# Optimization experiments

Measured on AMD Instinct MI355X. Metric: run time of the kernel, lower is better.

Reference implementation:

```python
import jax, jax.numpy as jnp
import numpy as np

H = 1024
B_SZ = 4
L = 2048


def setup_inputs() -> dict:
    key = jax.random.key(0)
    ks = jax.random.split(key, 7)
    s_in = 1.0 / np.sqrt(H)
    x = jax.random.normal(ks[0], (B_SZ, L, H), dtype=jnp.float32)
    # torch nn.Linear weights: (out_features, in_features)
    W_proj = jax.random.uniform(ks[1], (4 * H, H), minval=-s_in, maxval=s_in, dtype=jnp.float32)
    W_delta = jax.random.uniform(ks[2], (H, H), minval=-s_in, maxval=s_in, dtype=jnp.float32)
    b_delta = jax.random.uniform(ks[3], (H,), minval=-s_in, maxval=s_in, dtype=jnp.float32)
    A = 0.02 * jax.random.normal(ks[4], (1, 1, H), dtype=jnp.float32)
    Bp = 0.02 * jax.random.normal(ks[5], (1, H, 1), dtype=jnp.float32)
    D = jnp.ones((1,), dtype=jnp.float32)
    return {"x": x, "W_proj": W_proj, "A": A, "Bp": Bp, "D": D, "W_delta": W_delta, "b_delta": b_delta}


def reference(x, W_proj, A, Bp, D, W_delta, b_delta):
    # x: (b, l, h)
    h = x.shape[-1]
    proj = x @ W_proj.T                                   # (b, l, 4h)
    delta, Bs, Cs, residual = jnp.split(proj, 4, axis=-1) # each (b, l, h)
    delta = jax.nn.softplus(delta @ W_delta.T + b_delta)  # (b, l, h)
    A1 = A[0, 0]       # (h,)
    B1 = Bp[0, :, 0]   # (h,)
    # discretization: dA[b,h,l] = exp(delta*A)[b,l,h] * B1[h] (n-dim of Bp has size 1)
    dA = jnp.exp(delta * A1) * B1                         # (b, l, h), layout transposed vs torch
    # dB[b,h,0,l] = cumsum_l(delta[b,l,h] * B1[h])
    dB = jnp.cumsum(delta * B1, axis=1)                   # (b, l, h)
    # selective_scan: y[b,h,l] = sum_n (dA[b,h,l]*u[b,h,n] + dB[b,h,0,l]) * C[b,h,n]
    # sum over n distributes: y = dA * sum_n(u*C) + dB * sum_n(C)
    uC = jnp.sum(x * Cs, axis=1, keepdims=True)           # (b, 1, h)
    Csum = jnp.sum(Cs, axis=1, keepdims=True)             # (b, 1, h)
    y = dA * uC + dB * Csum                               # (b, l, h)
    return y + residual * D
```

## Files before the change

kernel.cpp:

```cpp
#include <hip/hip_runtime.h>
#include <hip/hip_bf16.h>
#include <cstdint>

#define H 1024
#define BSZ 4
#define LSEQ 2048
#define M_TOT (BSZ*LSEQ)
#define NCH2 128
#define LCH2 16

typedef __attribute__((ext_vector_type(4))) float  f32x4;
typedef __attribute__((ext_vector_type(2))) float  f32x2;
typedef __attribute__((ext_vector_type(8))) __bf16 bf16x8;
typedef __attribute__((ext_vector_type(4))) __bf16 bf16x4;
typedef __attribute__((ext_vector_type(2))) __bf16 bf16x2;

typedef __attribute__((address_space(1))) unsigned int as1_u32;
typedef __attribute__((address_space(3))) unsigned int as3_u32;

__device__ __forceinline__ void gld_lds16(const void* g, const void* l) {
    as1_u32* gp = reinterpret_cast<as1_u32*>((uintptr_t)g);
    as3_u32* lp = reinterpret_cast<as3_u32*>((uint32_t)(uintptr_t)l);
    __builtin_amdgcn_global_load_lds(gp, lp, 16, 0, 0);
}

__device__ __forceinline__ float softplus_fast(float f) {
    return fmaxf(f, 0.f) + __logf(1.f + __expf(-fabsf(f)));
}

#define BAR()    asm volatile("s_barrier" ::: "memory")
#define WAIT6()  asm volatile("s_waitcnt vmcnt(6)" ::: "memory")
#define WAIT0()  asm volatile("s_waitcnt vmcnt(0)" ::: "memory")

__global__ __launch_bounds__(256) void wfuse_gemm(
    const __bf16* __restrict__ A,
    const __bf16* __restrict__ B,
    __bf16* __restrict__ O)
{
    __shared__ __align__(16) __bf16 lds[2*4096];
    const int tid  = threadIdx.x;
    const int lane = tid & 63;
    const int wid  = tid >> 6;
    const int l15  = lane & 15;
    const int quad = lane >> 4;
    const int row0 = blockIdx.y * 64;
    const int col0 = blockIdx.x * 64;

    const __bf16* Asrc = A + (size_t)(row0 + (tid >> 2)) * 1024 + (tid & 3) * 8;
    const __bf16* Bsrc = B + (size_t)(col0 + (tid >> 2)) * 1024 + (tid & 3) * 8;
    const int ldst = (tid >> 2) * 32 + (tid & 3) * 8;

    auto stage = [&](int buf, int kt) {
        gld_lds16(Asrc + kt * 32, lds + buf * 4096 + ldst);
        gld_lds16(Bsrc + kt * 32, lds + buf * 4096 + 2048 + ldst);
    };

    f32x4 acc[4] = {};
    stage(0, 0);
#pragma unroll 2
    for (int kt = 0; kt < 32; ++kt) {
        __syncthreads();
        if (kt + 1 < 32) stage((kt + 1) & 1, kt + 1);
        const __bf16* base = lds + (kt & 1) * 4096;
        bf16x8 a = *(const bf16x8*)(base + (wid * 16 + l15) * 32 + quad * 8);
        bf16x8 b[4];
#pragma unroll
        for (int j = 0; j < 4; ++j)
            b[j] = *(const bf16x8*)(base + 2048 + (j * 16 + l15) * 32 + quad * 8);
#pragma unroll
        for (int j = 0; j < 4; ++j)
            acc[j] = __builtin_amdgcn_mfma_f32_16x16x32_bf16(a, b[j], acc[j], 0, 0, 0);
    }

    const int rowb = row0 + wid * 16 + quad * 4;
#pragma unroll
    for (int j = 0; j < 4; ++j) {
        const int col = col0 + j * 16 + l15;
#pragma unroll
        for (int r = 0; r < 4; ++r)
            O[(size_t)(rowb + r) * H + col] = (__bf16)acc[j][r];
    }
}


#define STA(b,u,kt) gld_lds16(Asrc + (size_t)((u)*64)*H + (kt)*64, \
                              lds + (b)*24576 + (u)*4096 + lwb)
#define STB(b,u,kt) gld_lds16(Bsrc + (size_t)((u)*64)*H + (kt)*64, \
                              lds + (b)*24576 + 16384 + (u)*4096 + lwb)
#define STAGE6(b,kt) do { STA(b,0,kt); STA(b,1,kt); STA(b,2,kt); STA(b,3,kt); \
                          STB(b,0,kt); STB(b,1,kt); } while(0)

#define TILE(bc,bn,kn,DS,WAITMAC) do {                                        \
    WAITMAC();                                                                \
    BAR();                                                                    \
    { const __bf16* base_ = lds + (bc)*24576;                                 \
      _Pragma("unroll")                                                       \
      for (int i_ = 0; i_ < 4; ++i_) {                                        \
          af0[i_] = *(const bf16x8*)(base_ + aoff[i_]);                       \
          bf0[i_] = *(const bf16x8*)(base_ + boff[i_]);                       \
      }                                                                       \
      _Pragma("unroll")                                                       \
      for (int i_ = 0; i_ < 4; ++i_) {                                        \
          af1[i_] = *(const bf16x8*)(base_ + (aoff[i_] ^ 32));                \
          bf1[i_] = *(const bf16x8*)(base_ + (boff[i_] ^ 32));                \
      } }                                                                     \
    if (DS) STAGE6(bn, kn);                                                   \
    __builtin_amdgcn_s_setprio(1);                                            \
    _Pragma("unroll")                                                         \
    for (int i_ = 0; i_ < 4; ++i_)                                            \
    _Pragma("unroll")                                                         \
    for (int j_ = 0; j_ < 4; ++j_)                                            \
        acc[i_][j_] = __builtin_amdgcn_mfma_f32_16x16x32_bf16(                \
            af0[i_], bf0[j_], acc[i_][j_], 0, 0, 0);                          \
    _Pragma("unroll")                                                         \
    for (int i_ = 0; i_ < 4; ++i_)                                            \
    _Pragma("unroll")                                                         \
    for (int j_ = 0; j_ < 4; ++j_)                                            \
        acc[i_][j_] = __builtin_amdgcn_mfma_f32_16x16x32_bf16(                \
            af1[i_], bf1[j_], acc[i_][j_], 0, 0, 0);                          \
    __builtin_amdgcn_s_setprio(0);                                            \
} while(0)

__global__ __launch_bounds__(512, 2) void gemm256b(
    const __bf16* __restrict__ A,
    const __bf16* __restrict__ B,
    __bf16* __restrict__ O0,
    __bf16* __restrict__ O2,
    const __bf16* __restrict__ xb,
    const float* __restrict__ bias,
    float* __restrict__ pD,
    float* __restrict__ pUp,
    float* __restrict__ pCp)
{
    __shared__ __align__(16) __bf16 lds[73728];

    const int tid  = threadIdx.x;
    const int lane = tid & 63;
    const int wid  = tid >> 6;
    const int l15  = lane & 15;
    const int quad = lane >> 4;
    const int wrv  = (wid >> 1) * 64;
    const int wcv  = (wid & 1) * 64;

    const int bid = blockIdx.x;
    const int swz = (bid & 7) * 96 + (bid >> 3);
    const int bx = swz % 24;
    const int by = swz / 24;
    const int row0 = by * 256;
    const int col0 = bx * 128;

    const int lg = (tid & 7) ^ ((tid >> 3) & 7);
    const __bf16* Asrc = A + (size_t)(row0 + (tid >> 3)) * H + lg * 8;
    const __bf16* Bsrc = B + (size_t)(col0 + (tid >> 3)) * H + lg * 8;
    const int lwb = wid * 512;

    int aoff[4], boff[4];
#pragma unroll
    for (int i = 0; i < 4; ++i)
        aoff[i] = (wrv + i*16 + l15)*64 + ((quad ^ (l15 & 7)) << 3);
#pragma unroll
    for (int j = 0; j < 4; ++j)
        boff[j] = 16384 + (wcv + j*16 + l15)*64 + ((quad ^ (l15 & 7)) << 3);

    f32x4 acc[4][4] = {};
    bf16x8 af0[4], bf0[4], af1[4], bf1[4];

    STAGE6(0, 0);
    STAGE6(1, 1);

#pragma unroll 1
    for (int g = 0; g < 4; ++g) {
        TILE(0, 2, 3*g + 2, 1, WAIT6);
        TILE(1, 0, 3*g + 3, 1, WAIT6);
        TILE(2, 1, 3*g + 4, 1, WAIT6);
    }
    TILE(0, 2, 14, 1, WAIT6);
    TILE(1, 0, 15, 1, WAIT6);
    TILE(2, 0,  0, 0, WAIT6);
    TILE(0, 0,  0, 0, WAIT0);
    __syncthreads();

    const int seg   = col0 >> 10;
    const int cbase = col0 & 1023;
    const int colb  = cbase + wcv + l15;
    const int rowb  = row0 + wrv + quad*4;

    if (seg == 0) {
        const int chunk16 = (row0 + wrv) >> 4;
#pragma unroll
        for (int j = 0; j < 4; ++j) {
            const int col = colb + j*16;
            const float bv = bias[col];
#pragma unroll
            for (int i = 0; i < 4; ++i) {
                float s = 0.f;
#pragma unroll
                for (int r = 0; r < 4; ++r) {
                    float f = softplus_fast(acc[i][j][r] + bv);
                    O0[(size_t)(rowb + i*16 + r) * H + col] = (__bf16)f;
                    s += f;
                }
                s += __shfl_down(s, 32); s += __shfl_down(s, 16);
                if (quad == 0) pD[(size_t)(chunk16 + i)*H + col] = s;
            }
        }
    } else if (seg == 2) {
#pragma unroll
        for (int i = 0; i < 4; ++i)
#pragma unroll
            for (int j = 0; j < 4; ++j) {
                const int col = colb + j*16;
#pragma unroll
                for (int r = 0; r < 4; ++r)
                    O2[(size_t)(rowb + i*16 + r) * H + col] = (__bf16)acc[i][j][r];
            }
    } else {
#pragma unroll
        for (int i = 0; i < 4; ++i)
#pragma unroll
            for (int j = 0; j < 4; ++j) {
                const int lcol = wcv + j*16 + l15;
#pragma unroll
                for (int r = 0; r < 4; ++r) {
                    const int lrow = wrv + i*16 + quad*4 + r;
                    lds[lrow*128 + (((lcol>>3) ^ (lrow&15)) << 3) + (lcol&7)]
                        = (__bf16)acc[i][j][r];
                }
            }
        __syncthreads();
        const int g = tid >> 4, oct = tid & 15;
        const int gc0 = cbase + oct*8;
        float su[8] = {}, sc[8] = {};
#pragma unroll
        for (int rr = 0; rr < 8; ++rr) {
            const int lrow = g*8 + rr;
            bf16x8 cv = *(const bf16x8*)(lds + lrow*128 +
                                         ((oct ^ (lrow&15)) << 3));
            bf16x8 xv = *(const bf16x8*)(xb + (size_t)(row0 + lrow)*H + gc0);
#pragma unroll
            for (int q = 0; q < 8; ++q) {
                float c = (float)cv[q];
                su[q] += (float)xv[q] * c;
                sc[q] += c;
            }
        }
        float* pf = reinterpret_cast<float*>(lds);
        __syncthreads();
#pragma unroll
        for (int q = 0; q < 8; ++q) {
            pf[g*128 + oct*8 + q]        = su[q];
            pf[4096 + g*128 + oct*8 + q] = sc[q];
        }
        __syncthreads();
        const int col = tid & 127;
        const int rb  = (tid >> 7) & 1;
        const int arr = tid >> 8;
        float s = 0.f;
#pragma unroll
        for (int g2 = 0; g2 < 16; ++g2)
            s += pf[arr*4096 + (rb*16 + g2)*128 + col];
        float* dst = arr ? pCp : pUp;
        dst[(size_t)((row0 >> 7) + rb)*H + cbase + col] = s;
    }
}

#define XB 8192
#define PB 2048
#define DB 1024
#define TB 256
__global__ void cast_kernel(const float* __restrict__ x,
                            const float* __restrict__ Wp,
                            const float* __restrict__ Wd,
                            __bf16* __restrict__ xb,
                            __bf16* __restrict__ Wpb,
                            __bf16* __restrict__ Wdb,
                            __bf16* __restrict__ Wp1T)
{
    __shared__ __bf16 tlds[64*65];
    const int t = threadIdx.x;
    const int bidx = blockIdx.x;

    if (bidx < XB + PB + DB) {
        const f32x4* src; __bf16* dst; int si, di;
        if (bidx < XB) {
            int i = bidx*256 + t;
            src = (const f32x4*)x;  si = i; dst = xb;  di = i;
        } else if (bidx < XB + PB) {
            int j = (bidx - XB)*256 + t;
            int row = j >> 8, cf = j & 255;
            src = (const f32x4*)Wp; si = (2048 + row)*256 + cf;
            dst = Wpb; di = (1024 + row)*256 + cf;
        } else {
            int j = (bidx - XB - PB)*256 + t;
            src = (const f32x4*)Wd; si = j; dst = Wdb; di = j;
        }
        f32x4 v = src[si];
        bf16x4 o = { (__bf16)v[0], (__bf16)v[1], (__bf16)v[2], (__bf16)v[3] };
        *(bf16x4*)(dst + (size_t)di*4) = o;
    } else {
        int tt = bidx - (XB + PB + DB);
        int ty = tt >> 4, tx = tt & 15;
        int rb = t >> 4, cb = t & 15;
#pragma unroll
        for (int rr = 0; rr < 4; ++rr) {
            int row = rb*4 + rr;
            f32x4 v = *(const f32x4*)(Wp + (size_t)(ty*64 + row)*1024 + tx*64 + cb*4);
#pragma unroll
            for (int q = 0; q < 4; ++q)
                tlds[row*65 + cb*4 + q] = (__bf16)v[q];
        }
        __syncthreads();
#pragma unroll
        for (int rr = 0; rr < 4; ++rr) {
            int kk = rb*4 + rr;
            bf16x4 o = { tlds[(cb*4+0)*65 + kk], tlds[(cb*4+1)*65 + kk],
                         tlds[(cb*4+2)*65 + kk], tlds[(cb*4+3)*65 + kk] };
            *(bf16x4*)(Wp1T + (size_t)(tx*64 + kk)*1024 + ty*64 + cb*4) = o;
        }
    }
}

__global__ __launch_bounds__(128) void final_kernel(
                             const __bf16* __restrict__ delta,
                             const __bf16* __restrict__ res,
                             const float* __restrict__ pD,
                             const float* __restrict__ pUp,
                             const float* __restrict__ pCp,
                             const float* __restrict__ Av,
                             const float* __restrict__ Bv,
                             const float* __restrict__ Dv,
                             float* __restrict__ out)
{
    const int c = blockIdx.x, b = blockIdx.z;
    const int h0 = blockIdx.y * 256 + threadIdx.x * 2;
    float run0 = 0.f, run1 = 0.f;
#pragma unroll 4
    for (int cp = 0; cp < c; ++cp) {
        f32x2 v = *(const f32x2*)(pD + (size_t)(b*NCH2 + cp)*H + h0);
        run0 += v[0]; run1 += v[1];
    }
    float uc0 = 0.f, uc1 = 0.f, cs0 = 0.f, cs1 = 0.f;
#pragma unroll
    for (int i = 0; i < 16; ++i) {
        f32x2 u = *(const f32x2*)(pUp + (b*16 + i)*H + h0);
        f32x2 s = *(const f32x2*)(pCp + (b*16 + i)*H + h0);
        uc0 += u[0]; uc1 += u[1]; cs0 += s[0]; cs1 += s[1];
    }
    const f32x2 a1 = *(const f32x2*)(Av + h0);
    const f32x2 b1 = *(const f32x2*)(Bv + h0);
    const float dd = Dv[0];
    size_t base = ((size_t)(b*LSEQ + c*LCH2)) * H + h0;
#pragma unroll 4
    for (int l = 0; l < LCH2; ++l) {
        size_t idx = base + (size_t)l * H;
        bf16x2 dv2 = *(const bf16x2*)(delta + idx);
        bf16x2 rs2 = *(const bf16x2*)(res + idx);
        float d0 = (float)dv2[0], d1v = (float)dv2[1];
        run0 += d0; run1 += d1v;
        f32x2 o;
        o[0] = __expf(d0*a1[0])*b1[0]*uc0 + run0*b1[0]*cs0 + (float)rs2[0]*dd;
        o[1] = __expf(d1v*a1[1])*b1[1]*uc1 + run1*b1[1]*cs1 + (float)rs2[1]*dd;
        *(f32x2*)(out + idx) = o;
    }
}

extern "C" void kernel_launch(void* const* d_in, const int* in_sizes, int n_in,
                              void* d_out, int out_size, void* d_ws, size_t ws_size,
                              hipStream_t stream)
{
    (void)in_sizes; (void)n_in; (void)out_size; (void)ws_size;
    const float* x  = (const float*)d_in[0];
    const float* Wp = (const float*)d_in[1];
    const float* Av = (const float*)d_in[2];
    const float* Bv = (const float*)d_in[3];
    const float* Dv = (const float*)d_in[4];
    const float* Wd = (const float*)d_in[5];
    const float* bd = (const float*)d_in[6];
    float* out = (float*)d_out;

    char* ws = (char*)d_ws;
    size_t o = 0;
    auto alloc = [&](size_t bytes) {
        void* p = ws + o; o += (bytes + 255) & ~(size_t)255; return p;
    };
    __bf16* xb   = (__bf16*)alloc((size_t)M_TOT * H * 2);
    __bf16* Wpb  = (__bf16*)alloc((size_t)3072 * H * 2);
    __bf16* Wdb  = (__bf16*)alloc((size_t)H * H * 2);
    __bf16* Wp1T = (__bf16*)alloc((size_t)H * H * 2);
    __bf16* resb = (__bf16*)alloc((size_t)M_TOT * H * 2);
    __bf16* db   = (__bf16*)alloc((size_t)M_TOT * H * 2);
    float*  pD   = (float*)alloc((size_t)BSZ * NCH2 * H * 4);
    float*  pUp  = (float*)alloc((size_t)64 * H * 4);
    float*  pCp  = (float*)alloc((size_t)64 * H * 4);

    cast_kernel<<<XB + PB + DB + TB, 256, 0, stream>>>(
        x, Wp, Wd, xb, Wpb, Wdb, Wp1T);
    wfuse_gemm<<<dim3(16, 16), 256, 0, stream>>>(Wdb, Wp1T, Wpb);
    gemm256b<<<dim3(768), 512, 0, stream>>>(
        xb, Wpb, db, resb, xb, bd, pD, pUp, pCp);
    final_kernel<<<dim3(NCH2, 4, BSZ), 128, 0, stream>>>(db, resb, pD, pUp, pCp,
                                                         Av, Bv, Dv, out);
}
```

Baseline: 192.9 us.

## Split K across wave pairs in GEMM with LDS reduction of partial accumulators

Reorganizes the 8-wave GEMM so each wave pair splits the 64-wide K slice in half, with every wave computing a 128x64 output subtile (8x4 MFMA tiles) over half of K. This gives more A/B fragment reuse per LDS read (12 fragment loads for 32 MFMAs instead of 16 for 32). At the end, the upper-K waves write their partial accumulators to LDS and the lower-K waves add them, and only those waves run the epilogue. The cost is double the accumulator registers (128 floats), which threatens occupancy at 2 blocks per CU, plus an extra LDS reduction pass and an epilogue that uses half the waves.

After: 214.8 us. 11.4% more time.

```diff
diff --git a/kernel.cpp b/kernel.cpp
--- a/kernel.cpp
+++ b/kernel.cpp
@@ -95,29 +95,19 @@
     BAR();                                                                    \
     { const __bf16* base_ = lds + (bc)*24576;                                 \
       _Pragma("unroll")                                                       \
-      for (int i_ = 0; i_ < 4; ++i_) {                                        \
-          af0[i_] = *(const bf16x8*)(base_ + aoff[i_]);                       \
-          bf0[i_] = *(const bf16x8*)(base_ + boff[i_]);                       \
-      }                                                                       \
+      for (int j_ = 0; j_ < 4; ++j_)                                          \
+          bf[j_] = *(const bf16x8*)(base_ + boff[j_]);                        \
       _Pragma("unroll")                                                       \
-      for (int i_ = 0; i_ < 4; ++i_) {                                        \
-          af1[i_] = *(const bf16x8*)(base_ + (aoff[i_] ^ 32));                \
-          bf1[i_] = *(const bf16x8*)(base_ + (boff[i_] ^ 32));                \
-      } }                                                                     \
+      for (int i_ = 0; i_ < 8; ++i_)                                          \
+          af[i_] = *(const bf16x8*)(base_ + aoff[i_]); }                      \
     if (DS) STAGE6(bn, kn);                                                   \
     __builtin_amdgcn_s_setprio(1);                                            \
     _Pragma("unroll")                                                         \
-    for (int i_ = 0; i_ < 4; ++i_)                                            \
+    for (int i_ = 0; i_ < 8; ++i_)                                            \
     _Pragma("unroll")                                                         \
     for (int j_ = 0; j_ < 4; ++j_)                                            \
         acc[i_][j_] = __builtin_amdgcn_mfma_f32_16x16x32_bf16(                \
-            af0[i_], bf0[j_], acc[i_][j_], 0, 0, 0);                          \
-    _Pragma("unroll")                                                         \
-    for (int i_ = 0; i_ < 4; ++i_)                                            \
-    _Pragma("unroll")                                                         \
-    for (int j_ = 0; j_ < 4; ++j_)                                            \
-        acc[i_][j_] = __builtin_amdgcn_mfma_f32_16x16x32_bf16(                \
-            af1[i_], bf1[j_], acc[i_][j_], 0, 0, 0);                          \
+            af[i_], bf[j_], acc[i_][j_], 0, 0, 0);                            \
     __builtin_amdgcn_s_setprio(0);                                            \
 } while(0)
 
@@ -139,8 +129,9 @@
     const int wid  = tid >> 6;
     const int l15  = lane & 15;
     const int quad = lane >> 4;
-    const int wrv  = (wid >> 1) * 64;
-    const int wcv  = (wid & 1) * 64;
+    const int kh = wid & 1;
+    const int nn = (wid >> 1) & 1;
+    const int mm = wid >> 2;
 
     const int bid = blockIdx.x;
     const int swz = (bid & 7) * 96 + (bid >> 3);
@@ -154,16 +145,16 @@
     const __bf16* Bsrc = B + (size_t)(col0 + (tid >> 3)) * H + lg * 8;
     const int lwb = wid * 512;
 
-    int aoff[4], boff[4];
-#pragma unroll
-    for (int i = 0; i < 4; ++i)
-        aoff[i] = (wrv + i*16 + l15)*64 + ((quad ^ (l15 & 7)) << 3);
+    int aoff[8], boff[4];
+#pragma unroll
+    for (int i = 0; i < 8; ++i)
+        aoff[i] = (mm*128 + i*16 + l15)*64 + (((kh*4 + quad) ^ (l15 & 7)) << 3);
 #pragma unroll
     for (int j = 0; j < 4; ++j)
-        boff[j] = 16384 + (wcv + j*16 + l15)*64 + ((quad ^ (l15 & 7)) << 3);
-
-    f32x4 acc[4][4] = {};
-    bf16x8 af0[4], bf0[4], af1[4], bf1[4];
+        boff[j] = 16384 + (nn*64 + j*16 + l15)*64 + (((kh*4 + quad) ^ (l15 & 7)) << 3);
+
+    f32x4 acc[8][4] = {};
+    bf16x8 af[8], bf[4];
 
     STAGE6(0, 0);
     STAGE6(1, 1);
@@ -180,53 +171,81 @@
     TILE(0, 0,  0, 0, WAIT0);
     __syncthreads();
 
+    float* pf = reinterpret_cast<float*>(lds);
+    const int pairb = (wid >> 1) * 8192;
+    if (kh == 1) {
+#pragma unroll
+        for (int i = 0; i < 8; ++i)
+#pragma unroll
+            for (int j = 0; j < 4; ++j)
+                *(f32x4*)(pf + pairb + (i*4 + j)*256 + lane*4) = acc[i][j];
+    }
+    __syncthreads();
+    if (kh == 0) {
+#pragma unroll
+        for (int i = 0; i < 8; ++i)
+#pragma unroll
+            for (int j = 0; j < 4; ++j) {
+                f32x4 v = *(const f32x4*)(pf + pairb + (i*4 + j)*256 + lane*4);
+                acc[i][j][0] += v[0]; acc[i][j][1] += v[1];
+                acc[i][j][2] += v[2]; acc[i][j][3] += v[3];
+            }
+    }
+
     const int seg   = col0 >> 10;
     const int cbase = col0 & 1023;
-    const int colb  = cbase + wcv + l15;
-    const int rowb  = row0 + wrv + quad*4;
+    const int colb  = cbase + nn*64 + l15;
+    const int rowb  = row0 + mm*128 + quad*4;
 
     if (seg == 0) {
-        const int chunk16 = (row0 + wrv) >> 4;
-#pragma unroll
-        for (int j = 0; j < 4; ++j) {
-            const int col = colb + j*16;
-            const float bv = bias[col];
-#pragma unroll
-            for (int i = 0; i < 4; ++i) {
-                float s = 0.f;
-#pragma unroll
-                for (int r = 0; r < 4; ++r) {
-                    float f = softplus_fast(acc[i][j][r] + bv);
-                    O0[(size_t)(rowb + i*16 + r) * H + col] = (__bf16)f;
-                    s += f;
-                }
-                s += __shfl_down(s, 32); s += __shfl_down(s, 16);
-                if (quad == 0) pD[(size_t)(chunk16 + i)*H + col] = s;
-            }
-        }
-    } else if (seg == 2) {
-#pragma unroll
-        for (int i = 0; i < 4; ++i)
+        if (kh == 0) {
+            const int chunk16 = (row0 + mm*128) >> 4;
 #pragma unroll
             for (int j = 0; j < 4; ++j) {
                 const int col = colb + j*16;
-#pragma unroll
-                for (int r = 0; r < 4; ++r)
-                    O2[(size_t)(rowb + i*16 + r) * H + col] = (__bf16)acc[i][j][r];
-            }
-    } else {
-#pragma unroll
-        for (int i = 0; i < 4; ++i)
-#pragma unroll
-            for (int j = 0; j < 4; ++j) {
-                const int lcol = wcv + j*16 + l15;
-#pragma unroll
-                for (int r = 0; r < 4; ++r) {
-                    const int lrow = wrv + i*16 + quad*4 + r;
-                    lds[lrow*128 + (((lcol>>3) ^ (lrow&15)) << 3) + (lcol&7)]
-                        = (__bf16)acc[i][j][r];
+                const float bv = bias[col];
+#pragma unroll
+                for (int i = 0; i < 8; ++i) {
+                    float s = 0.f;
+#pragma unroll
+                    for (int r = 0; r < 4; ++r) {
+                        float f = softplus_fast(acc[i][j][r] + bv);
+                        O0[(size_t)(rowb + i*16 + r) * H + col] = (__bf16)f;
+                        s += f;
+                    }
+                    s += __shfl_down(s, 32); s += __shfl_down(s, 16);
+                    if (quad == 0) pD[(size_t)(chunk16 + i)*H + col] = s;
                 }
             }
+        }
+    } else if (seg == 2) {
+        if (kh == 0) {
+#pragma unroll
+            for (int i = 0; i < 8; ++i)
+#pragma unroll
+                for (int j = 0; j < 4; ++j) {
+                    const int col = colb + j*16;
+#pragma unroll
+                    for (int r = 0; r < 4; ++r)
+                        O2[(size_t)(rowb + i*16 + r) * H + col] = (__bf16)acc[i][j][r];
+                }
+        }
+    } else {
+        __syncthreads();
+        if (kh == 0) {
+#pragma unroll
+            for (int i = 0; i < 8; ++i)
+#pragma unroll
+                for (int j = 0; j < 4; ++j) {
+                    const int lcol = nn*64 + j*16 + l15;
+#pragma unroll
+                    for (int r = 0; r < 4; ++r) {
+                        const int lrow = mm*128 + i*16 + quad*4 + r;
+                        lds[lrow*128 + (((lcol>>3) ^ (lrow&15)) << 3) + (lcol&7)]
+                            = (__bf16)acc[i][j][r];
+                    }
+                }
+        }
         __syncthreads();
         const int g = tid >> 4, oct = tid & 15;
         const int gc0 = cbase + oct*8;
@@ -244,7 +263,6 @@
                 sc[q] += c;
             }
         }
-        float* pf = reinterpret_cast<float*>(lds);
         __syncthreads();
 #pragma unroll
         for (int q = 0; q < 8; ++q) {
```

## Load B operand directly into registers, staging only A through LDS

Applied to the files above, without the earlier changes.

The main GEMM now streams only the A tile through a triple-buffered LDS pipeline. The B fragments are loaded straight from global memory into two ping-pong register sets, one k-step ahead. This cuts LDS size (and possibly raises occupancy) and removes the B LDS reads and their bank traffic. In exchange it adds register pressure, and it relies on uncoalesced per-wave global loads of B whose latency is covered only by the vmcnt waits.

Result: slower. 268.6 us (+39.3%).

```diff
diff --git a/kernel.cpp b/kernel.cpp
--- a/kernel.cpp
+++ b/kernel.cpp
@@ -29,7 +29,7 @@
 }
 
 #define BAR()    asm volatile("s_barrier" ::: "memory")
-#define WAIT6()  asm volatile("s_waitcnt vmcnt(6)" ::: "memory")
+#define WAIT4()  asm volatile("s_waitcnt vmcnt(4)" ::: "memory")
 #define WAIT0()  asm volatile("s_waitcnt vmcnt(0)" ::: "memory")
 
 __global__ __launch_bounds__(256) void wfuse_gemm(
@@ -83,41 +83,46 @@
 }
 
 
-#define STA(b,u,kt) gld_lds16(Asrc + (size_t)((u)*64)*H + (kt)*64, \
-                              lds + (b)*24576 + (u)*4096 + lwb)
-#define STB(b,u,kt) gld_lds16(Bsrc + (size_t)((u)*64)*H + (kt)*64, \
-                              lds + (b)*24576 + 16384 + (u)*4096 + lwb)
-#define STAGE6(b,kt) do { STA(b,0,kt); STA(b,1,kt); STA(b,2,kt); STA(b,3,kt); \
-                          STB(b,0,kt); STB(b,1,kt); } while(0)
-
-#define TILE(bc,bn,kn,DS,WAITMAC) do {                                        \
+#define STA4(b,kt) do {                                                       \
+    gld_lds16(Asrc + (size_t)  0*H + (kt)*64, lds + (b)*16384 +         lwb); \
+    gld_lds16(Asrc + (size_t) 64*H + (kt)*64, lds + (b)*16384 +  4096 + lwb); \
+    gld_lds16(Asrc + (size_t)128*H + (kt)*64, lds + (b)*16384 +  8192 + lwb); \
+    gld_lds16(Asrc + (size_t)192*H + (kt)*64, lds + (b)*16384 + 12288 + lwb); \
+} while(0)
+
+#define BLOAD(dst, kt) do {                                                   \
+    _Pragma("unroll")                                                         \
+    for (int j_ = 0; j_ < 4; ++j_) {                                          \
+        dst[j_]     = *(const bf16x8*)(Bpj[j_] + (kt)*64);                    \
+        dst[4 + j_] = *(const bf16x8*)(Bpj[j_] + (kt)*64 + 32);               \
+    }                                                                         \
+} while(0)
+
+#define TILEB(bc,bn,kn, BC, BN, knB, DB_, DS, WAITMAC) do {                   \
     WAITMAC();                                                                \
     BAR();                                                                    \
-    { const __bf16* base_ = lds + (bc)*24576;                                 \
+    { const __bf16* base_ = lds + (bc)*16384;                                 \
       _Pragma("unroll")                                                       \
       for (int i_ = 0; i_ < 4; ++i_) {                                        \
           af0[i_] = *(const bf16x8*)(base_ + aoff[i_]);                       \
-          bf0[i_] = *(const bf16x8*)(base_ + boff[i_]);                       \
-      }                                                                       \
-      _Pragma("unroll")                                                       \
-      for (int i_ = 0; i_ < 4; ++i_) {                                        \
           af1[i_] = *(const bf16x8*)(base_ + (aoff[i_] ^ 32));                \
-          bf1[i_] = *(const bf16x8*)(base_ + (boff[i_] ^ 32));                \
       } }                                                                     \
-    if (DS) STAGE6(bn, kn);                                                   \
+    if (DB_) BLOAD(BN, knB);                                                  \
+    asm volatile("" ::: "memory");   \
+    if (DS) STA4(bn, kn);                                                     \
     __builtin_amdgcn_s_setprio(1);                                            \
     _Pragma("unroll")                                                         \
     for (int i_ = 0; i_ < 4; ++i_)                                            \
     _Pragma("unroll")                                                         \
     for (int j_ = 0; j_ < 4; ++j_)                                            \
         acc[i_][j_] = __builtin_amdgcn_mfma_f32_16x16x32_bf16(                \
-            af0[i_], bf0[j_], acc[i_][j_], 0, 0, 0);                          \
+            af0[i_], BC[j_], acc[i_][j_], 0, 0, 0);                           \
     _Pragma("unroll")                                                         \
     for (int i_ = 0; i_ < 4; ++i_)                                            \
     _Pragma("unroll")                                                         \
     for (int j_ = 0; j_ < 4; ++j_)                                            \
         acc[i_][j_] = __builtin_amdgcn_mfma_f32_16x16x32_bf16(                \
-            af1[i_], bf1[j_], acc[i_][j_], 0, 0, 0);                          \
+            af1[i_], BC[4 + j_], acc[i_][j_], 0, 0, 0);                       \
     __builtin_amdgcn_s_setprio(0);                                            \
 } while(0)
 
@@ -132,7 +137,7 @@
     float* __restrict__ pUp,
     float* __restrict__ pCp)
 {
-    __shared__ __align__(16) __bf16 lds[73728];
+    __shared__ __align__(16) __bf16 lds[49152];
 
     const int tid  = threadIdx.x;
     const int lane = tid & 63;
@@ -151,33 +156,39 @@
 
     const int lg = (tid & 7) ^ ((tid >> 3) & 7);
     const __bf16* Asrc = A + (size_t)(row0 + (tid >> 3)) * H + lg * 8;
-    const __bf16* Bsrc = B + (size_t)(col0 + (tid >> 3)) * H + lg * 8;
     const int lwb = wid * 512;
 
-    int aoff[4], boff[4];
+    int aoff[4];
 #pragma unroll
     for (int i = 0; i < 4; ++i)
         aoff[i] = (wrv + i*16 + l15)*64 + ((quad ^ (l15 & 7)) << 3);
-#pragma unroll
-    for (int j = 0; j < 4; ++j)
-        boff[j] = 16384 + (wcv + j*16 + l15)*64 + ((quad ^ (l15 & 7)) << 3);
+
+    const __bf16* Bp0 = B + (size_t)(col0 + wcv + l15) * H + quad*8;
+    const __bf16* Bpj[4] = { Bp0, Bp0 + 16*H, Bp0 + 32*H, Bp0 + 48*H };
 
     f32x4 acc[4][4] = {};
-    bf16x8 af0[4], bf0[4], af1[4], bf1[4];
-
-    STAGE6(0, 0);
-    STAGE6(1, 1);
+    bf16x8 af0[4], af1[4];
+    bf16x8 bfP[8], bfQ[8];
+
+    STA4(0, 0);
+    asm volatile("" ::: "memory");
+    BLOAD(bfP, 0);
+    asm volatile("" ::: "memory");
+    STA4(1, 1);
 
 #pragma unroll 1
-    for (int g = 0; g < 4; ++g) {
-        TILE(0, 2, 3*g + 2, 1, WAIT6);
-        TILE(1, 0, 3*g + 3, 1, WAIT6);
-        TILE(2, 1, 3*g + 4, 1, WAIT6);
-    }
-    TILE(0, 2, 14, 1, WAIT6);
-    TILE(1, 0, 15, 1, WAIT6);
-    TILE(2, 0,  0, 0, WAIT6);
-    TILE(0, 0,  0, 0, WAIT0);
+    for (int g = 0; g < 2; ++g) {
+        TILEB(0, 2, 6*g + 2, bfP, bfQ, 6*g + 1, 1, 1, WAIT4);
+        TILEB(1, 0, 6*g + 3, bfQ, bfP, 6*g + 2, 1, 1, WAIT4);
+        TILEB(2, 1, 6*g + 4, bfP, bfQ, 6*g + 3, 1, 1, WAIT4);
+        TILEB(0, 2, 6*g + 5, bfQ, bfP, 6*g + 4, 1, 1, WAIT4);
+        TILEB(1, 0, 6*g + 6, bfP, bfQ, 6*g + 5, 1, 1, WAIT4);
+        TILEB(2, 1, 6*g + 7, bfQ, bfP, 6*g + 6, 1, 1, WAIT4);
+    }
+    TILEB(0, 2, 14, bfP, bfQ, 13, 1, 1, WAIT4);
+    TILEB(1, 0, 15, bfQ, bfP, 14, 1, 1, WAIT4);
+    TILEB(2, 0,  0, bfP, bfQ, 15, 1, 0, WAIT4);
+    TILEB(0, 0,  0, bfQ, bfP,  0, 0, 0, WAIT0);
     __syncthreads();
 
     const int seg   = col0 >> 10;
```
